# Kernel optimization log

Hardware: AMD Instinct MI355X
Metric: run time of the kernel (lower is better)

The kernel has to match this reference:

```python
import jax, jax.numpy as jnp
import numpy as np
import math

L = 2          # gnn_num_layers
NDIM = 256     # gnn_hidden_size
H = 8          # num_heads
HH = H // 2    # heads per (full, local) split
DK = NDIM // H # 32, also == edim (relation_share_heads)
EDIM = DK
B, NPB = 32, 128
N = B * NPB            # 4096 nodes
EF = B * NPB * NPB     # 524288 complete-graph edges
EL = 131072            # local-graph edges
ELG = 262144           # line-graph edges
R = 128                # relation vocab


def _ln(x, g, b, eps=1e-5):
    m = x.mean(-1, keepdims=True)
    v = ((x - m) ** 2).mean(-1, keepdims=True)
    return (x - m) / jnp.sqrt(v + eps) * g + b


def _ffn(x, W1, b1, W2, b2, g, b):
    h = jax.nn.relu(x @ W1 + b1)
    return _ln(x + h @ W2 + b2, g, b)


def _edge_attn(q, k, v, e, src, dst, n_seg):
    """Relation-aware graph attention (DGL propagate_attention + edge_softmax).
    q,k,v: [n_seg,h,d]; e: [E,h,d] edge-relation bias or None; src,dst: [E].
    score_e = ((k[src]+e) . q[dst]) / sqrt(d); softmax over in-edges of dst;
    out[dst] = sum alpha_e * (v[src]+e)."""
    ks = k[src] + e if e is not None else k[src]          # [E,h,d]
    vs = v[src] + e if e is not None else v[src]          # [E,h,d]
    s = jnp.einsum('ehd,ehd->eh', ks, q[dst]) / math.sqrt(q.shape[-1])
    smax = jax.ops.segment_max(s, dst, num_segments=n_seg)
    ex = jnp.exp(s - jnp.maximum(smax, -1e30)[dst])
    den = jax.ops.segment_sum(ex, dst, num_segments=n_seg)[dst]
    alpha = ex / jnp.where(den > 0, den, 1.0)
    return jax.ops.segment_sum(alpha[..., None] * vs, dst, num_segments=n_seg)


def _model(x, rel_embed,
           n_Wq, n_bq, n_Wk, n_bk, n_Wv, n_bv, n_Wo, n_bo, n_ln_g, n_ln_b,
           n_f_W1, n_f_b1, n_f_W2, n_f_b2, n_f_ln_g, n_f_ln_b,
           e_Wsrc, e_Wdst, e_Wq, e_bq, e_Wk, e_Wv, e_Wo, e_bo, e_ln_g, e_ln_b,
           e_f_W1, e_f_b1, e_f_W2, e_f_b2, e_f_ln_g, e_f_ln_b,
           full_src, full_dst, g_src, g_dst, lg_src, lg_dst, edge_feat, full_edge_feat):
    lg_x = rel_embed[edge_feat]            # [EL, EDIM]  (shared embedding)
    lg_x_full = rel_embed[full_edge_feat]  # [EF, EDIM]  (fixed across layers)
    n, el, ef = x.shape[0], lg_x.shape[0], lg_x_full.shape[0]
    for i in range(L):
        # ---------- node update: first HH heads on full graph, last HH on local ----------
        q = (x @ n_Wq[i] + n_bq[i]).reshape(n, H, DK)
        k = (x @ n_Wk[i] + n_bk[i]).reshape(n, H, DK)
        v = (x @ n_Wv[i] + n_bv[i]).reshape(n, H, DK)
        # edim == d_k -> relation bias broadcast across heads (the expand branch)
        e_full = jnp.broadcast_to(lg_x_full[:, None, :], (ef, HH, DK))
        e_loc = jnp.broadcast_to(lg_x[:, None, :], (el, HH, DK))
        o1 = _edge_attn(q[:, :HH], k[:, :HH], v[:, :HH], e_full, full_src, full_dst, n)
        o2 = _edge_attn(q[:, HH:], k[:, HH:], v[:, HH:], e_loc, g_src, g_dst, n)
        o = jnp.concatenate([o1, o2], axis=1).reshape(n, NDIM)
        x_new = _ln(x + o @ n_Wo[i] + n_bo[i], n_ln_g[i], n_ln_b[i])
        x_new = _ffn(x_new, n_f_W1[i], n_f_b1[i], n_f_W2[i], n_f_b2[i], n_f_ln_g[i], n_f_ln_b[i])
        # ---------- edge update on line graph, conditioned on PRE-update src/dst node feats ----------
        mixed = lg_x + x[g_src] @ e_Wsrc[i] + x[g_dst] @ e_Wdst[i]  # [EL, EDIM]
        dke = EDIM // H
        eq = (mixed @ e_Wq[i] + e_bq[i]).reshape(el, H, dke)
        ek = (mixed @ e_Wk[i]).reshape(el, H, dke)
        ev = (mixed @ e_Wv[i]).reshape(el, H, dke)
        ow = _edge_attn(eq, ek, ev, None, lg_src, lg_dst, el).reshape(el, EDIM)
        lg_new = _ln(lg_x + ow @ e_Wo[i] + e_bo[i], e_ln_g[i], e_ln_b[i])
        lg_new = _ffn(lg_new, e_f_W1[i], e_f_b1[i], e_f_W2[i], e_f_b2[i], e_f_ln_g[i], e_f_ln_b[i])
        x, lg_x = x_new, lg_new
    return x, lg_x


def setup_inputs() -> dict:
    key = jax.random.key(0)
    ki = iter(jax.random.split(key, 48))
    def p(shape, scale=0.05):
        return jax.random.normal(next(ki), shape, dtype=jnp.float32) * scale
    rng = np.random.default_rng(0)
    blk = (np.arange(B, dtype=np.int32) * NPB)
    ii, jj = np.meshgrid(np.arange(NPB, dtype=np.int32), np.arange(NPB, dtype=np.int32), indexing='ij')
    full_src = (blk[:, None, None] + ii[None]).reshape(-1)   # block-diagonal complete graph
    full_dst = (blk[:, None, None] + jj[None]).reshape(-1)
    epb = EL // B
    g_src = (np.repeat(blk, epb) + rng.integers(0, NPB, EL)).astype(np.int32)
    g_dst = (np.repeat(blk, epb) + rng.integers(0, NPB, EL)).astype(np.int32)
    lpb = ELG // B
    eblk = np.arange(B, dtype=np.int32) * epb
    lg_src = (np.repeat(eblk, lpb) + rng.integers(0, epb, ELG)).astype(np.int32)
    lg_dst = (np.repeat(eblk, lpb) + rng.integers(0, epb, ELG)).astype(np.int32)
    return dict(
        x=jax.random.normal(next(ki), (N, NDIM), dtype=jnp.float32),
        rel_embed=p((R, EDIM), 1.0),
        full_src=jnp.asarray(full_src), full_dst=jnp.asarray(full_dst),
        g_src=jnp.asarray(g_src), g_dst=jnp.asarray(g_dst),
        lg_src=jnp.asarray(lg_src), lg_dst=jnp.asarray(lg_dst),
        edge_feat=jnp.asarray(rng.integers(0, R, EL).astype(np.int32)),
        full_edge_feat=jnp.asarray(rng.integers(0, R, EF).astype(np.int32)),
        n_Wq=p((L, NDIM, NDIM)), n_bq=p((L, NDIM)),
        n_Wk=p((L, NDIM, NDIM)), n_bk=p((L, NDIM)),
        n_Wv=p((L, NDIM, NDIM)), n_bv=p((L, NDIM)),
        n_Wo=p((L, NDIM, NDIM)), n_bo=p((L, NDIM)),
        n_ln_g=jnp.ones((L, NDIM), jnp.float32), n_ln_b=jnp.zeros((L, NDIM), jnp.float32),
        n_f_W1=p((L, NDIM, 4 * NDIM)), n_f_b1=p((L, 4 * NDIM)),
        n_f_W2=p((L, 4 * NDIM, NDIM)), n_f_b2=p((L, NDIM)),
        n_f_ln_g=jnp.ones((L, NDIM), jnp.float32), n_f_ln_b=jnp.zeros((L, NDIM), jnp.float32),
        e_Wsrc=p((L, NDIM, EDIM)), e_Wdst=p((L, NDIM, EDIM)),
        e_Wq=p((L, EDIM, EDIM)), e_bq=p((L, EDIM)),
        e_Wk=p((L, EDIM, EDIM)), e_Wv=p((L, EDIM, EDIM)),
        e_Wo=p((L, EDIM, EDIM)), e_bo=p((L, EDIM)),
        e_ln_g=jnp.ones((L, EDIM), jnp.float32), e_ln_b=jnp.zeros((L, EDIM), jnp.float32),
        e_f_W1=p((L, EDIM, 4 * EDIM)), e_f_b1=p((L, 4 * EDIM)),
        e_f_W2=p((L, 4 * EDIM, EDIM)), e_f_b2=p((L, EDIM)),
        e_f_ln_g=jnp.ones((L, EDIM), jnp.float32), e_f_ln_b=jnp.zeros((L, EDIM), jnp.float32),
    )


def reference(x, rel_embed, full_src, full_dst, g_src, g_dst, lg_src, lg_dst,
              edge_feat, full_edge_feat,
              n_Wq, n_bq, n_Wk, n_bk, n_Wv, n_bv, n_Wo, n_bo, n_ln_g, n_ln_b,
              n_f_W1, n_f_b1, n_f_W2, n_f_b2, n_f_ln_g, n_f_ln_b,
              e_Wsrc, e_Wdst, e_Wq, e_bq, e_Wk, e_Wv, e_Wo, e_bo, e_ln_g, e_ln_b,
              e_f_W1, e_f_b1, e_f_W2, e_f_b2, e_f_ln_g, e_f_ln_b):
    return _model(x, rel_embed,
                  n_Wq, n_bq, n_Wk, n_bk, n_Wv, n_bv, n_Wo, n_bo, n_ln_g, n_ln_b,
                  n_f_W1, n_f_b1, n_f_W2, n_f_b2, n_f_ln_g, n_f_ln_b,
                  e_Wsrc, e_Wdst, e_Wq, e_bq, e_Wk, e_Wv, e_Wo, e_bo, e_ln_g, e_ln_b,
                  e_f_W1, e_f_b1, e_f_W2, e_f_b2, e_f_ln_g, e_f_ln_b,
                  full_src, full_dst, g_src, g_dst, lg_src, lg_dst, edge_feat, full_edge_feat)
```

## Files before the change

kernel.cpp:

```cpp
#include <hip/hip_runtime.h>
#include <hip/hip_bf16.h>

typedef __hip_bfloat16 bf16;
typedef unsigned short ush;

static constexpr int kN   = 4096;
static constexpr int kND  = 256;
static constexpr int kEL  = 131072;
static constexpr int kED  = 32;
static constexpr int kELG = 262144;
static constexpr int kL   = 2;
static constexpr int kQW  = 832;
static constexpr float kScaleN = 0.17677669529663687f;

using frag_ab = __attribute__((ext_vector_type(8))) short;
using frag_cd = __attribute__((ext_vector_type(4))) float;

__device__ __forceinline__ float ldf(const void* p, size_t i, int isbf){
    return isbf ? __bfloat162float(((const bf16*)p)[i]) : ((const float*)p)[i];
}
__device__ __forceinline__ ush f2b(float f){ bf16 h = __float2bfloat16(f); return *(ush*)&h; }
__device__ __forceinline__ float b2f(ush u){ return __uint_as_float(((unsigned)u)<<16); }
__device__ __forceinline__ ush ldb(const void* p, size_t i, int isbf){
    return isbf ? ((const ush*)p)[i] : f2b(((const float*)p)[i]);
}

__global__ void detect_k(const ush* __restrict__ xin, int* __restrict__ flag){
    if (threadIdx.x == 0 && blockIdx.x == 0) {
        int plausible = 0;
        for (int i = 0; i < 128; ++i) {
            ush u = xin[i];
            int e = (u >> 7) & 0xFF;
            if (e == 0 || (e >= 110 && e <= 140)) ++plausible;
        }
        *flag = (plausible >= 102) ? 1 : 0;
    }
}

__global__ void setup_misc_k(const void* __restrict__ xin, const void* __restrict__ rel,
                             const int* __restrict__ feat,
                             const void* __restrict__ bq, const void* __restrict__ bk,
                             const void* __restrict__ bv,
                             float* __restrict__ xA, float* __restrict__ lgA,
                             float* __restrict__ bQKV,
                             int* __restrict__ cntL, int* __restrict__ cntG,
                             const int* __restrict__ flag){
    const int isbf = *flag;
    long g = (long)blockIdx.x*256 + threadIdx.x;
    if (g < (long)kN*kND) { xA[g] = ldf(xin, g, isbf); return; }
    g -= (long)kN*kND;
    if (g < (long)kEL*kED) { int e = (int)(g >> 5), d = (int)(g & 31);
        lgA[g] = ldf(rel, (size_t)feat[e]*kED + d, isbf); return; }
    g -= (long)kEL*kED;
    if (g < 2*kQW) {
        int layer = (int)(g / kQW), j = (int)(g - (long)layer*kQW);
        float v = 0.f;
        if (j < 768) { int w = j >> 8, jj = j & 255;
            const void* B = (w==0)?bq:((w==1)?bk:bv);
            v = ldf(B, (size_t)layer*256 + jj, isbf); }
        bQKV[g] = v; return;
    }
    g -= 2*kQW;
    if (g < kN) { cntL[g] = 0; return; }
    g -= kN;
    if (g < kEL) { cntG[g] = 0; return; }
}

__global__ void trans_all_k(
    const void* __restrict__ nWq, const void* __restrict__ nWk, const void* __restrict__ nWv,
    const void* __restrict__ nWo, const void* __restrict__ nF1, const void* __restrict__ nF2,
    const void* __restrict__ eWs, const void* __restrict__ eWd,
    const void* __restrict__ eWq, const void* __restrict__ eWk, const void* __restrict__ eWv,
    const void* __restrict__ eWo, const void* __restrict__ eF1, const void* __restrict__ eF2,
    const int* __restrict__ flag,
    ush* __restrict__ wtQKVSD, ush* __restrict__ wtO, ush* __restrict__ wtF1,
    ush* __restrict__ wtF2, ush* __restrict__ wtEQKV, ush* __restrict__ wtEO,
    ush* __restrict__ wtEF1, ush* __restrict__ wtEF2)
{
    const int isbf = *flag;
    int g = blockIdx.x*256 + threadIdx.x;
    if (g < 393216){
        int w = g >> 17, gg = g & 131071;
        int layer = gg >> 16, idx = gg & 65535;
        int n = idx >> 8, k = idx & 255;
        const void* W = (w==0)?nWq:((w==1)?nWk:nWv);
        wtQKVSD[(size_t)layer*212992 + (size_t)(w*256+n)*256 + k] =
            ldb(W, (size_t)layer*65536 + (size_t)k*256 + n, isbf);
        return;
    }
    g -= 393216;
    if (g < 32768){
        int w = g >> 14, gg = g & 16383;
        int layer = gg >> 13, idx = gg & 8191;
        int n = idx >> 8, k = idx & 255;
        const void* W = w ? eWd : eWs;
        wtQKVSD[(size_t)layer*212992 + (size_t)(768 + w*32 + n)*256 + k] =
            ldb(W, (size_t)layer*8192 + (size_t)k*32 + n, isbf);
        return;
    }
    g -= 32768;
    if (g < 131072){
        int layer = g >> 16, rem = g & 65535;
        int n = rem >> 8, k = rem & 255;
        wtO[g] = ldb(nWo, (size_t)layer*65536 + (size_t)k*256 + n, isbf);
        return;
    }
    g -= 131072;
    if (g < 524288){
        int layer = g >> 18, rem = g & 262143;
        int n = rem >> 8, k = rem & 255;
        wtF1[g] = ldb(nF1, (size_t)layer*262144 + (size_t)k*1024 + n, isbf);
        return;
    }
    g -= 524288;
    if (g < 524288){
        int layer = g >> 18, rem = g & 262143;
        int n = rem >> 10, k = rem & 1023;
        wtF2[g] = ldb(nF2, (size_t)layer*262144 + (size_t)k*256 + n, isbf);
        return;
    }
    g -= 524288;
    if (g < 6144){
        int w = g >> 11, gg = g & 2047;
        int layer = gg >> 10, rem = gg & 1023;
        int n = rem >> 5, k = rem & 31;
        const void* W = (w==0)?eWq:((w==1)?eWk:eWv);
        wtEQKV[g] = ldb(W, (size_t)layer*1024 + (size_t)k*32 + n, isbf);
        return;
    }
    g -= 6144;
    if (g < 2048){
        int layer = g >> 10, rem = g & 1023;
        int n = rem >> 5, k = rem & 31;
        wtEO[g] = ldb(eWo, (size_t)layer*1024 + (size_t)k*32 + n, isbf);
        return;
    }
    g -= 2048;
    if (g < 8192){
        int layer = g >> 12, rem = g & 4095;
        int n = rem >> 5, k = rem & 31;
        wtEF1[g] = ldb(eF1, (size_t)layer*4096 + (size_t)k*128 + n, isbf);
        return;
    }
    g -= 8192;
    if (g < 8192){
        int layer = g >> 12, rem = g & 4095;
        int n = rem >> 7, k = rem & 127;
        wtEF2[g] = ldb(eF2, (size_t)layer*4096 + (size_t)k*32 + n, isbf);
        return;
    }
}

__global__ void count2_k(const int* __restrict__ gd, const int* __restrict__ lgd,
                         int* __restrict__ cntL, int* __restrict__ cntG){
    int g = blockIdx.x*256 + threadIdx.x;
    if (g < kEL) atomicAdd(&cntL[gd[g]], 1);
    else if (g < kEL + kELG) atomicAdd(&cntG[lgd[g - kEL]], 1);
}
__global__ __launch_bounds__(256) void scan_blk2_k(
    const int* __restrict__ cntL, const int* __restrict__ cntG,
    int* __restrict__ rowL, int* __restrict__ rowG, int* __restrict__ bsum)
{
    __shared__ int s[256];
    const int t = threadIdx.x;
    const bool isL = blockIdx.x < 4;
    const int* cnt = isL ? cntL : cntG;
    int* out = isL ? rowL : rowG;
    const int blk = isL ? blockIdx.x : blockIdx.x - 4;
    const int n = isL ? kN : kEL;
    const int b0 = blk*1024;
    int v[4], pre[4], tsum = 0;
    #pragma unroll
    for (int j=0;j<4;++j){
        int idx = b0 + t*4 + j;
        v[j] = (idx < n) ? cnt[idx] : 0;
        pre[j] = tsum; tsum += v[j];
    }
    s[t] = tsum; __syncthreads();
    for (int off=1; off<256; off<<=1){
        int x = (t>=off) ? s[t-off] : 0;
        __syncthreads();
        s[t] += x;
        __syncthreads();
    }
    int texc = s[t] - tsum;
    #pragma unroll
    for (int j=0;j<4;++j){
        int idx = b0 + t*4 + j;
        if (idx < n) out[idx] = texc + pre[j];
    }
    if (t == 255) bsum[(isL ? 0 : 8) + blk] = s[255];
}
__global__ __launch_bounds__(256) void scan_top2_k(int* __restrict__ bsum){
    __shared__ int sL[256], sG[256];
    const int t = threadIdx.x;
    int vL = (t < 4)   ? bsum[t]     : 0;
    int vG = (t < 128) ? bsum[8 + t] : 0;
    sL[t] = vL; sG[t] = vG; __syncthreads();
    for (int off=1; off<256; off<<=1){
        int xL = (t>=off) ? sL[t-off] : 0;
        int xG = (t>=off) ? sG[t-off] : 0;
        __syncthreads();
        sL[t] += xL; sG[t] += xG;
        __syncthreads();
    }
    if (t < 4)   bsum[t]     = sL[t] - vL;
    if (t < 128) bsum[8 + t] = sG[t] - vG;
}
__global__ void scan_add2_k(int* __restrict__ rowL, int* __restrict__ rowG,
                            const int* __restrict__ bsum,
                            int* __restrict__ curL, int* __restrict__ curG){
    int g = blockIdx.x*256 + threadIdx.x;
    if (g < kN){ int v = rowL[g] + bsum[g >> 10]; rowL[g] = v; curL[g] = v; }
    else if (g < kN + kEL){ int gg = g - kN;
        int v = rowG[gg] + bsum[8 + (gg >> 10)]; rowG[gg] = v; curG[gg] = v; }
    if (g == 0){ rowL[kN] = kEL; rowG[kEL] = kELG; }
}
__global__ void fill2_k(const int* __restrict__ gd, const int* __restrict__ lgd,
                        int* __restrict__ curL, int* __restrict__ curG,
                        int* __restrict__ eidL, int* __restrict__ eidG){
    int g = blockIdx.x*256 + threadIdx.x;
    if (g < kEL){ int pos = atomicAdd(&curL[gd[g]], 1); eidL[pos] = g; }
    else if (g < kEL + kELG){ int gg = g - kEL;
        int pos = atomicAdd(&curG[lgd[gg]], 1); eidG[pos] = gg; }
}

__global__ __launch_bounds__(256) void mgemm_k(
    const float* __restrict__ A, const ush* __restrict__ WT,
    const void* __restrict__ bias, size_t boff,
    float* __restrict__ C, const int* __restrict__ flag,
    int M, int N, int K, int flags)
{
    __shared__ __align__(16) ush As[64*40];
    __shared__ __align__(16) ush Ws[64*40];
    const int isbf = *flag;
    const int t = threadIdx.x;
    const int m0 = blockIdx.y*64, n0 = blockIdx.x*64;
    const int wave = t>>6, lane = t&63;
    const int quad = lane>>4, l15 = lane&15;
    const int r = t>>2, kq = (t&3)*8;
    const bool abf = flags & 32;

    frag_cd acc[4];
    #pragma unroll
    for (int tl=0; tl<4; ++tl)
        #pragma unroll
        for (int j=0;j<4;++j) acc[tl][j] = 0.f;

    const float* aprow = A + (size_t)(m0+r)*K + kq;
    const ush*   abrow = (const ush*)A + (size_t)(m0+r)*K + kq;
    const bool wok = (n0 + r) < N;
    const ush* wprow = WT + (size_t)(n0 + (wok ? r : 0))*K + kq;

    float4 a0, a1; uint4 av; uint4 wv;
    auto loadT = [&](int kk){
        if (abf) av = *(const uint4*)(abrow + kk);
        else { a0 = *(const float4*)(aprow + kk); a1 = *(const float4*)(aprow + kk + 4); }
        wv = wok ? *(const uint4*)(wprow + kk) : make_uint4(0u,0u,0u,0u);
    };
    loadT(0);

    for (int kk = 0; kk < K; kk += 32) {
        if (abf) {
            *(uint4*)&As[r*40 + kq] = av;
        } else {
            ushort4 p0 = make_ushort4(f2b(a0.x), f2b(a0.y), f2b(a0.z), f2b(a0.w));
            ushort4 p1 = make_ushort4(f2b(a1.x), f2b(a1.y), f2b(a1.z), f2b(a1.w));
            *(ushort4*)&As[r*40 + kq]     = p0;
            *(ushort4*)&As[r*40 + kq + 4] = p1;
        }
        *(uint4*)&Ws[r*40 + kq] = wv;
        __syncthreads();
        if (kk + 32 < K) loadT(kk + 32);
        frag_ab af = *(const frag_ab*)&As[(wave*16 + l15)*40 + quad*8];
        #pragma unroll
        for (int tl = 0; tl < 4; ++tl) {
            frag_ab bf = *(const frag_ab*)&Ws[(tl*16 + l15)*40 + quad*8];
            acc[tl] = __builtin_amdgcn_mfma_f32_16x16x32_bf16(af, bf, acc[tl], 0, 0, 0);
        }
        __syncthreads();
    }
    const bool do_relu = flags & 2;
    const bool has_b   = flags & 4;
    const bool obf     = flags & 8;
    #pragma unroll
    for (int tl = 0; tl < 4; ++tl) {
        int col = n0 + tl*16 + l15;
        if (col < N) {
            float bv = 0.f;
            if (has_b) bv = (flags & 16) ? ((const float*)bias)[boff + col]
                                         : ldf(bias, boff + col, isbf);
            #pragma unroll
            for (int rg = 0; rg < 4; ++rg) {
                int row = m0 + wave*16 + quad*4 + rg;
                float v = acc[tl][rg] + bv;
                if (do_relu) v = fmaxf(v, 0.f);
                if (obf) ((ush*)C)[(size_t)row*N + col] = f2b(v);
                else     C[(size_t)row*N + col] = v;
            }
        }
    }
}

__global__ __launch_bounds__(64) void ln_k(
    const float* __restrict__ a, const float* __restrict__ b,
    const void* __restrict__ g, const void* __restrict__ be, size_t goff,
    float* __restrict__ out, const int* __restrict__ flag, int D)
{
    const int isbf = *flag;
    const int row = blockIdx.x;
    const int t = threadIdx.x;
    float v[4];
    int cnt = 0;
    float s = 0.f;
    for (int i = t; i < D; i += 64) {
        float x = a[(size_t)row*D + i];
        if (b) x += b[(size_t)row*D + i];
        v[cnt++] = x; s += x;
    }
    #pragma unroll
    for (int off = 32; off > 0; off >>= 1) s += __shfl_down(s, off);
    s = __shfl(s, 0);
    const float mean = s / D;
    float qq = 0.f;
    for (int c2 = 0; c2 < cnt; ++c2) { float d = v[c2]-mean; qq += d*d; }
    #pragma unroll
    for (int off = 32; off > 0; off >>= 1) qq += __shfl_down(qq, off);
    qq = __shfl(qq, 0);
    const float inv = rsqrtf(fmaxf(qq, 0.f) / D + 1e-5f);
    cnt = 0;
    for (int i = t; i < D; i += 64)
        out[(size_t)row*D + i] = (v[cnt++] - mean)*inv*ldf(g, goff + i, isbf) + ldf(be, goff + i, isbf);
}

__global__ __launch_bounds__(256) void eqkv_mfma_k(
    const float* __restrict__ lg, const float* __restrict__ xsd,
    const int* __restrict__ gsrc, const int* __restrict__ gdst,
    const ush* __restrict__ WQKV, size_t woff,
    const void* __restrict__ bq, size_t boff,
    ush* __restrict__ eq, ush* __restrict__ ek, ush* __restrict__ ev,
    const int* __restrict__ flag)
{
    __shared__ __align__(16) ush mixs[128*40];
    __shared__ __align__(16) ush wts[3][32*40];
    __shared__ float bqs[32];
    const int isbf = *flag;
    const int t = threadIdx.x;
    const int e0 = blockIdx.x * 128;
    #pragma unroll
    for (int i = t; i < 768; i += 256) {
        int m = i >> 8, r2 = i & 255;
        int n = r2 >> 3, k4 = (r2 & 7) * 4;
        *(ushort4*)&wts[m][n*40 + k4] =
            *(const ushort4*)&WQKV[(size_t)m*2048 + woff + (size_t)n*32 + k4];
    }
    if (t < 32) bqs[t] = ldf(bq, boff + t, isbf);
    {
        int r = t >> 1, c0 = (t & 1) * 16;
        int e = e0 + r;
        int s = gsrc[e], d2 = gdst[e];
        const float* lp = lg + (size_t)e*32 + c0;
        const float* sp = xsd + (size_t)s*kQW + c0;
        const float* dp = xsd + (size_t)d2*kQW + 32 + c0;
        #pragma unroll
        for (int j = 0; j < 16; ++j)
            mixs[r*40 + c0 + j] = f2b(lp[j] + sp[j] + dp[j]);
    }
    __syncthreads();
    const int wave = t >> 6, l15 = t & 15, quad = (t >> 4) & 3;
    #pragma unroll
    for (int mi = 0; mi < 2; ++mi) {
        const int mt = wave*2 + mi;
        frag_ab af = *(const frag_ab*)&mixs[(mt*16 + l15)*40 + quad*8];
        #pragma unroll
        for (int w = 0; w < 3; ++w) {
            ush* outp = (w==0) ? eq : ((w==1) ? ek : ev);
            #pragma unroll
            for (int nt = 0; nt < 2; ++nt) {
                frag_ab bf = *(const frag_ab*)&wts[w][(nt*16 + l15)*40 + quad*8];
                frag_cd acc = {0.f, 0.f, 0.f, 0.f};
                acc = __builtin_amdgcn_mfma_f32_16x16x32_bf16(af, bf, acc, 0, 0, 0);
                const float bv = (w==0) ? bqs[nt*16 + l15] : 0.f;
                #pragma unroll
                for (int rg = 0; rg < 4; ++rg) {
                    int row = e0 + mt*16 + quad*4 + rg;
                    outp[(size_t)row*32 + nt*16 + l15] = f2b(acc[rg] + bv);
                }
            }
        }
    }
}

__global__ __launch_bounds__(256) void effn_mfma_k(
    const float* __restrict__ A,
    const ush* __restrict__ W1T, size_t w1off, const void* __restrict__ b1, size_t b1off,
    const ush* __restrict__ W2T, size_t w2off, const void* __restrict__ b2, size_t b2off,
    const void* __restrict__ g, const void* __restrict__ be, size_t goff,
    float* __restrict__ out, const int* __restrict__ flag)
{
    __shared__ __align__(16) ush w1t[128*40];
    __shared__ __align__(16) ush w2t[32*136];
    __shared__ __align__(16) ush hid[64*136];
    __shared__ float b1s[128], b2s[32];
    const int isbf = *flag;
    const int t = threadIdx.x;
    const int wave = t >> 6, l15 = t & 15, quad = (t >> 4) & 3;

    #pragma unroll
    for (int i = t; i < 1024; i += 256) {
        int n1 = i >> 3, k4 = (i & 7) * 4;
        *(ushort4*)&w1t[n1*40 + k4] = *(const ushort4*)&W1T[w1off + (size_t)n1*32 + k4];
        int n2 = i >> 5, kq2 = (i & 31) * 4;
        *(ushort4*)&w2t[n2*136 + kq2] = *(const ushort4*)&W2T[w2off + (size_t)n2*128 + kq2];
    }
    if (t < 128) b1s[t] = ldf(b1, b1off + t, isbf);
    if (t < 32)  b2s[t] = ldf(b2, b2off + t, isbf);
    __syncthreads();

    const float g0  = ldf(g,  goff + l15, isbf),      g1v = ldf(g,  goff + 16 + l15, isbf);
    const float be0 = ldf(be, goff + l15, isbf),      be1 = ldf(be, goff + 16 + l15, isbf);
    const float bb0 = b2s[l15], bb1 = b2s[16 + l15];

    for (int tt = 0; tt < 2; ++tt) {
        const int e0 = (blockIdx.x*2 + tt) * 64;
        {
            const int m = wave*16 + l15;
            float4 a0 = *(const float4*)&A[(size_t)(e0+m)*32 + quad*8];
            float4 a1 = *(const float4*)&A[(size_t)(e0+m)*32 + quad*8 + 4];
            ush tmp[8] = {f2b(a0.x),f2b(a0.y),f2b(a0.z),f2b(a0.w),
                          f2b(a1.x),f2b(a1.y),f2b(a1.z),f2b(a1.w)};
            frag_ab af = *(frag_ab*)tmp;
            #pragma unroll
            for (int nt = 0; nt < 8; ++nt) {
                frag_ab bf = *(const frag_ab*)&w1t[(nt*16 + l15)*40 + quad*8];
                frag_cd acc = {0.f, 0.f, 0.f, 0.f};
                acc = __builtin_amdgcn_mfma_f32_16x16x32_bf16(af, bf, acc, 0, 0, 0);
                float bv = b1s[nt*16 + l15];
                #pragma unroll
                for (int rg = 0; rg < 4; ++rg) {
                    int row = wave*16 + quad*4 + rg;
                    hid[row*136 + nt*16 + l15] = f2b(fmaxf(acc[rg] + bv, 0.f));
                }
            }
        }
        frag_cd acc2[2] = {{0.f,0.f,0.f,0.f},{0.f,0.f,0.f,0.f}};
        #pragma unroll
        for (int ks = 0; ks < 4; ++ks) {
            frag_ab af2 = *(const frag_ab*)&hid[(wave*16 + l15)*136 + ks*32 + quad*8];
            #pragma unroll
            for (int tl = 0; tl < 2; ++tl) {
                frag_ab bf2 = *(const frag_ab*)&w2t[(tl*16 + l15)*136 + ks*32 + quad*8];
                acc2[tl] = __builtin_amdgcn_mfma_f32_16x16x32_bf16(af2, bf2, acc2[tl], 0, 0, 0);
            }
        }
        #pragma unroll
        for (int rg = 0; rg < 4; ++rg) {
            const int row = e0 + wave*16 + quad*4 + rg;
            float v0 = acc2[0][rg] + bb0 + A[(size_t)row*32 + l15];
            float v1 = acc2[1][rg] + bb1 + A[(size_t)row*32 + 16 + l15];
            float s = v0 + v1;
            s += __shfl_xor(s,1); s += __shfl_xor(s,2); s += __shfl_xor(s,4); s += __shfl_xor(s,8);
            const float mean = s * (1.f/32.f);
            float q = (v0-mean)*(v0-mean) + (v1-mean)*(v1-mean);
            q += __shfl_xor(q,1); q += __shfl_xor(q,2); q += __shfl_xor(q,4); q += __shfl_xor(q,8);
            const float inv = rsqrtf(q * (1.f/32.f) + 1e-5f);
            out[(size_t)row*32 + l15]      = (v0-mean)*inv*g0  + be0;
            out[(size_t)row*32 + 16 + l15] = (v1-mean)*inv*g1v + be1;
        }
    }
}

__global__ __launch_bounds__(512) void full_attn_k(
    const float* __restrict__ q, const float* __restrict__ k, const float* __restrict__ v,
    const void* __restrict__ rel, const int* __restrict__ feat, float* __restrict__ o,
    const int* __restrict__ flag, int ldq)
{
    __shared__ __align__(8) ush ks[128][36];
    __shared__ __align__(8) ush vs[128][36];
    __shared__ __align__(8) ush rs[128][36];
    __shared__ float pb[8][32][34];
    const int isbf = *flag;
    const int bid = blockIdx.x;
    const int b = bid >> 4, h = (bid >> 2) & 3, qtr = bid & 3;
    const int t = threadIdx.x;
    for (int i = t; i < 4096; i += 512) {
        int r = i >> 5, d = i & 31;
        rs[r][d] = ldb(rel, i, isbf);
        size_t base = ((size_t)(b*128 + r))*ldq + h*32 + d;
        ks[r][d] = f2b(k[base]);
        vs[r][d] = f2b(v[base]);
    }
    __syncthreads();
    const int wave = t >> 6, lane = t & 63;
    const int dstL = lane >> 1, part = lane & 1;
    const int dst = qtr*32 + dstL;
    const int dbase = part*16;
    float qr[16];
    { size_t base = ((size_t)(b*128 + dst))*ldq + h*32 + dbase;
      #pragma unroll
      for (int d=0; d<16; ++d) qr[d] = q[base + d]; }
    const int* fp = feat + (size_t)b*16384 + dst;
    const int s0 = wave*16;
    float m = -1e30f, l = 0.f;
    float acc[16];
    #pragma unroll
    for (int d=0; d<16; ++d) acc[d] = 0.f;
    int f = fp[s0*128];
    for (int sI = 0; sI < 16; ++sI) {
        const int s = s0 + sI;
        int fn = (sI+1 < 16) ? fp[(s+1)*128] : 0;
        float er[16];
        float scp = 0.f;
        #pragma unroll
        for (int j2 = 0; j2 < 4; ++j2) {
            ushort4 eu = *(const ushort4*)&rs[f][dbase + j2*4];
            ushort4 ku = *(const ushort4*)&ks[s][dbase + j2*4];
            float e0 = b2f(eu.x), e1 = b2f(eu.y), e2 = b2f(eu.z), e3 = b2f(eu.w);
            er[j2*4+0]=e0; er[j2*4+1]=e1; er[j2*4+2]=e2; er[j2*4+3]=e3;
            scp += (b2f(ku.x)+e0)*qr[j2*4+0] + (b2f(ku.y)+e1)*qr[j2*4+1]
                 + (b2f(ku.z)+e2)*qr[j2*4+2] + (b2f(ku.w)+e3)*qr[j2*4+3];
        }
        const float sc = (scp + __shfl_xor(scp, 1)) * kScaleN;
        float mn = fmaxf(m, sc);
        float c0 = __expf(m - mn);
        float pp = __expf(sc - mn);
        l = l*c0 + pp;
        #pragma unroll
        for (int j2 = 0; j2 < 4; ++j2) {
            ushort4 vu = *(const ushort4*)&vs[s][dbase + j2*4];
            acc[j2*4+0] = acc[j2*4+0]*c0 + pp*(b2f(vu.x)+er[j2*4+0]);
            acc[j2*4+1] = acc[j2*4+1]*c0 + pp*(b2f(vu.y)+er[j2*4+1]);
            acc[j2*4+2] = acc[j2*4+2]*c0 + pp*(b2f(vu.z)+er[j2*4+2]);
            acc[j2*4+3] = acc[j2*4+3]*c0 + pp*(b2f(vu.w)+er[j2*4+3]);
        }
        m = mn; f = fn;
    }
    if (part == 0) { pb[wave][dstL][0] = m; pb[wave][dstL][1] = l; }
    #pragma unroll
    for (int d=0; d<16; ++d) pb[wave][dstL][2 + dbase + d] = acc[d];
    __syncthreads();
    {
        const int dstL2 = t & 31, grp = t >> 5;
        float mw[8], lw[8];
        #pragma unroll
        for (int w=0; w<8; ++w){ mw[w]=pb[w][dstL2][0]; lw[w]=pb[w][dstL2][1]; }
        float M = mw[0];
        #pragma unroll
        for (int w=1; w<8; ++w) M = fmaxf(M, mw[w]);
        float sw[8];
        float L = 0.f;
        #pragma unroll
        for (int w=0; w<8; ++w){ sw[w] = __expf(mw[w]-M); L += lw[w]*sw[w]; }
        const float inv = 1.f / fmaxf(L, 1e-30f);
        size_t base = ((size_t)(b*128 + qtr*32 + dstL2))*kND + h*32 + grp*2;
        #pragma unroll
        for (int d=0; d<2; ++d) {
            float a = 0.f;
            #pragma unroll
            for (int w=0; w<8; ++w) a += pb[w][dstL2][2+grp*2+d]*sw[w];
            o[base + d] = a*inv;
        }
    }
}

__global__ __launch_bounds__(256) void loc_gather_k(
    const float* __restrict__ q, const float* __restrict__ k, const float* __restrict__ v,
    const float* __restrict__ lg, const int* __restrict__ gsrc,
    const int* __restrict__ rowp, const int* __restrict__ eidl,
    float* __restrict__ o, int ldq)
{
    const int n = blockIdx.x;
    const int h = threadIdx.x >> 6;
    const int lane = threadIdx.x & 63;
    const int g = lane >> 4;
    const int d0 = (lane & 15) * 2;
    const size_t hoff = (size_t)(4 + h) * 32 + d0;
    const float2 q2 = *(const float2*)&q[(size_t)n*ldq + hoff];
    const int beg = rowp[n], end = rowp[n+1];
    const int deg = end - beg;
    float m = -1e30f, l = 0.f, ax = 0.f, ay = 0.f;
    if (deg > 0) {
        const int nIter = (deg + 3) >> 2;
        int idx = beg + g;
        int ce = eidl[min(idx, end-1)];
        int cs = gsrc[ce];
        for (int it = 0; it < nIter; ++it) {
            const bool valid = idx < end;
            const int e = ce, s = cs;
            idx += 4;
            if (it + 1 < nIter) { ce = eidl[min(idx, end-1)]; cs = gsrc[ce]; }
            const float2 kv = *(const float2*)&k[(size_t)s*ldq + hoff];
            const float2 lv = *(const float2*)&lg[(size_t)e*32 + d0];
            const float2 vv = *(const float2*)&v[(size_t)s*ldq + hoff];
            float part = (kv.x+lv.x)*q2.x + (kv.y+lv.y)*q2.y;
            part += __shfl_xor(part, 1);
            part += __shfl_xor(part, 2);
            part += __shfl_xor(part, 4);
            part += __shfl_xor(part, 8);
            const float sc = part * kScaleN;
            const float mn = valid ? fmaxf(m, sc) : m;
            const float c  = __expf(m - mn);
            const float pp = valid ? __expf(sc - mn) : 0.f;
            l  = l*c  + pp;
            ax = ax*c + pp*(vv.x+lv.x);
            ay = ay*c + pp*(vv.y+lv.y);
            m  = mn;
        }
        #pragma unroll
        for (int off = 16; off <= 32; off <<= 1) {
            const float mo = __shfl_xor(m, off);
            const float lo = __shfl_xor(l, off);
            const float xo = __shfl_xor(ax, off);
            const float yo = __shfl_xor(ay, off);
            const float M  = fmaxf(m, mo);
            const float c1 = __expf(m - M);
            const float c2 = __expf(mo - M);
            l  = l*c1  + lo*c2;
            ax = ax*c1 + xo*c2;
            ay = ay*c1 + yo*c2;
            m  = M;
        }
    }
    if (g == 0) {
        const float inv = 1.f / fmaxf(l, 1e-30f);
        *(float2*)&o[(size_t)n*kND + hoff] = make_float2(ax*inv, ay*inv);
    }
}

__global__ __launch_bounds__(256) void lgs_ewo_k(
    const ush* __restrict__ eq, const ush* __restrict__ ek, const ush* __restrict__ ev,
    const int* __restrict__ lsrc, const int* __restrict__ rowp, const int* __restrict__ eidl,
    const float* __restrict__ res,
    const ush* __restrict__ WO, size_t wooff, const void* __restrict__ bo, size_t booff,
    const void* __restrict__ g1, const void* __restrict__ be1, size_t g1off,
    float* __restrict__ out, const int* __restrict__ flag)
{
    __shared__ __align__(16) ush ows[32*40];
    __shared__ __align__(16) ush wos[32*40];
    __shared__ float cs[32][36];
    __shared__ float bos[32], gs[32], bs[32];
    const int isbf = *flag;
    const int t = threadIdx.x;
    const int base = blockIdx.x * 32;
    {
        int n = t >> 3, k4 = (t & 7) * 4;
        *(ushort4*)&wos[n*40 + k4] = *(const ushort4*)&WO[wooff + (size_t)n*32 + k4];
    }
    if (t < 32) {
        bos[t] = ldf(bo, booff + t, isbf);
        gs[t]  = ldf(g1, g1off + t, isbf);
        bs[t]  = ldf(be1, g1off + t, isbf);
    }
    {
        const int d2 = base + (t >> 3), h = t & 7;
        const ushort4 qu = *(const ushort4*)&eq[(size_t)d2*32 + h*4];
        const float q0 = b2f(qu.x), q1 = b2f(qu.y), q2 = b2f(qu.z), q3 = b2f(qu.w);
        const int beg = rowp[d2], end = rowp[d2+1];
        float m = -1e30f, l = 0.f;
        float4 acc = make_float4(0.f,0.f,0.f,0.f);
        int i = beg;
        int s = 0;
        if (i < end) { s = lsrc[eidl[i]]; }
        while (i < end) {
            const int sc_s = s;
            ++i;
            if (i < end) { s = lsrc[eidl[i]]; }
            const ushort4 ku = *(const ushort4*)&ek[(size_t)sc_s*32 + h*4];
            const ushort4 vu = *(const ushort4*)&ev[(size_t)sc_s*32 + h*4];
            float sc = (b2f(ku.x)*q0 + b2f(ku.y)*q1 + b2f(ku.z)*q2 + b2f(ku.w)*q3) * 0.5f;
            float mn = fmaxf(m, sc);
            float c = __expf(m - mn);
            float pp = __expf(sc - mn);
            l = l*c + pp;
            acc.x = acc.x*c + pp*b2f(vu.x);
            acc.y = acc.y*c + pp*b2f(vu.y);
            acc.z = acc.z*c + pp*b2f(vu.z);
            acc.w = acc.w*c + pp*b2f(vu.w);
            m = mn;
        }
        const float inv = 1.f / fmaxf(l, 1e-30f);
        const int r = t >> 3, c0 = h*4;
        ows[r*40 + c0 + 0] = f2b(acc.x*inv);
        ows[r*40 + c0 + 1] = f2b(acc.y*inv);
        ows[r*40 + c0 + 2] = f2b(acc.z*inv);
        ows[r*40 + c0 + 3] = f2b(acc.w*inv);
    }
    __syncthreads();
    {
        const int wave = t >> 6, l15 = t & 15, quad = (t >> 4) & 3;
        const int mt = wave & 1, nt = wave >> 1;
        frag_ab af = *(const frag_ab*)&ows[(mt*16 + l15)*40 + quad*8];
        frag_ab bf = *(const frag_ab*)&wos[(nt*16 + l15)*40 + quad*8];
        frag_cd acc = {0.f, 0.f, 0.f, 0.f};
        acc = __builtin_amdgcn_mfma_f32_16x16x32_bf16(af, bf, acc, 0, 0, 0);
        #pragma unroll
        for (int rg = 0; rg < 4; ++rg) {
            const int row = mt*16 + quad*4 + rg;
            const int col = nt*16 + l15;
            cs[row][col] = acc[rg] + bos[col] + res[(size_t)(base+row)*32 + col];
        }
    }
    __syncthreads();
    {
        const int row = t >> 3, c0 = (t & 7) * 4;
        const float v0 = cs[row][c0], v1 = cs[row][c0+1];
        const float v2 = cs[row][c0+2], v3 = cs[row][c0+3];
        float s = v0+v1+v2+v3;
        s += __shfl_xor(s,1); s += __shfl_xor(s,2); s += __shfl_xor(s,4);
        const float mean = s * (1.f/32.f);
        float qq = (v0-mean)*(v0-mean)+(v1-mean)*(v1-mean)
                 + (v2-mean)*(v2-mean)+(v3-mean)*(v3-mean);
        qq += __shfl_xor(qq,1); qq += __shfl_xor(qq,2); qq += __shfl_xor(qq,4);
        const float inv = rsqrtf(qq * (1.f/32.f) + 1e-5f);
        float o0 = (v0-mean)*inv*gs[c0+0] + bs[c0+0];
        float o1 = (v1-mean)*inv*gs[c0+1] + bs[c0+1];
        float o2 = (v2-mean)*inv*gs[c0+2] + bs[c0+2];
        float o3 = (v3-mean)*inv*gs[c0+3] + bs[c0+3];
        *(float4*)&out[(size_t)(base+row)*32 + c0] = make_float4(o0,o1,o2,o3);
    }
}

__global__ void out_k(const float* __restrict__ xf, const float* __restrict__ lgf,
                      void* __restrict__ out, const int* __restrict__ flag){
    const int isbf = *flag;
    int g = blockIdx.x*256 + threadIdx.x;
    float v = (g < kN*kND) ? xf[g] : lgf[g - kN*kND];
    if (isbf) ((bf16*)out)[g] = __float2bfloat16(v);
    else      ((float*)out)[g] = v;
}

static inline void mgemm(const float* A, const ush* WT, const void* bias, size_t boff,
                         float* C, const int* flag, int M, int N, int K, int flags,
                         hipStream_t s){
    dim3 grid((N+63)/64, M/64);
    mgemm_k<<<grid, 256, 0, s>>>(A, WT, bias, boff, C, flag, M, N, K, flags);
}

extern "C" void kernel_launch(void* const* d_in, const int* in_sizes, int n_in,
                              void* d_out, int out_size, void* d_ws, size_t ws_size,
                              hipStream_t stream) {
    const void* x_in      = d_in[0];
    const void* rel       = d_in[1];
    const int* g_src      = (const int*)d_in[4];
    const int* g_dst      = (const int*)d_in[5];
    const int* lg_src     = (const int*)d_in[6];
    const int* lg_dst     = (const int*)d_in[7];
    const int* edge_feat  = (const int*)d_in[8];
    const int* full_feat  = (const int*)d_in[9];
    const void* n_Wq   = d_in[10];
    const void* n_bq   = d_in[11];
    const void* n_Wk   = d_in[12];
    const void* n_bk   = d_in[13];
    const void* n_Wv   = d_in[14];
    const void* n_bv   = d_in[15];
    const void* n_Wo   = d_in[16];
    const void* n_bo   = d_in[17];
    const void* n_lng  = d_in[18];
    const void* n_lnb  = d_in[19];
    const void* n_fW1  = d_in[20];
    const void* n_fb1  = d_in[21];
    const void* n_fW2  = d_in[22];
    const void* n_fb2  = d_in[23];
    const void* n_flng = d_in[24];
    const void* n_flnb = d_in[25];
    const void* e_Wsrc = d_in[26];
    const void* e_Wdst = d_in[27];
    const void* e_Wq   = d_in[28];
    const void* e_bq   = d_in[29];
    const void* e_Wk   = d_in[30];
    const void* e_Wv   = d_in[31];
    const void* e_Wo   = d_in[32];
    const void* e_bo   = d_in[33];
    const void* e_lng  = d_in[34];
    const void* e_lnb  = d_in[35];
    const void* e_fW1  = d_in[36];
    const void* e_fb1  = d_in[37];
    const void* e_fW2  = d_in[38];
    const void* e_fb2  = d_in[39];
    const void* e_flng = d_in[40];
    const void* e_flnb = d_in[41];

    float* p = (float*)d_ws;
    size_t off = 0;
    auto AL = [&](size_t n){ float* r = p + off; off += n; return r; };
    int* flagp = (int*)AL(64);
    float* xA   = AL((size_t)kN*kND);
    float* xB   = AL((size_t)kN*kND);
    float* xM   = AL((size_t)kN*kND);
    float* qkvb = AL((size_t)kN*kQW);
    float* ob   = AL((size_t)kN*kND);
    float* tN   = AL((size_t)kN*kND);
    ush*   nh   = (ush*)AL((size_t)kN*512);
    float* lgA  = AL((size_t)kEL*kED);
    float* lgB  = AL((size_t)kEL*kED);
    float* lgM  = AL((size_t)kEL*kED);
    ush*   eqb  = (ush*)AL((size_t)kEL*16);
    ush*   ekb  = (ush*)AL((size_t)kEL*16);
    ush*   evb  = (ush*)AL((size_t)kEL*16);
    int* cntL  = (int*)AL(kN);
    int* rowL  = (int*)AL(kN + 64);
    int* curL  = (int*)AL(kN);
    int* eidL  = (int*)AL(kEL);
    int* cntG  = (int*)AL(kEL);
    int* rowG  = (int*)AL(kEL + 64);
    int* curG  = (int*)AL(kEL);
    int* eidG  = (int*)AL(kELG);
    int* bsum  = (int*)AL(256);
    ush* wtQKVSD = (ush*)AL(212992);
    float* bQKV  = AL(2*kQW);
    ush* wtO  = (ush*)AL(65536);
    ush* wtF1 = (ush*)AL(262144);
    ush* wtF2 = (ush*)AL(262144);
    ush* wtEQKV = (ush*)AL(3072);
    ush* wtEO   = (ush*)AL(1024);
    ush* wtEF1  = (ush*)AL(4096);
    ush* wtEF2  = (ush*)AL(4096);
    if (ws_size < off * sizeof(float)) return;

    detect_k<<<1, 64, 0, stream>>>((const ush*)x_in, flagp);
    {
        long total = (long)kN*kND + (long)kEL*kED + 2*kQW + kN + kEL;
        int blocks = (int)((total + 255) / 256);
        setup_misc_k<<<blocks, 256, 0, stream>>>(x_in, rel, edge_feat, n_bq, n_bk, n_bv,
                                                 xA, lgA, bQKV, cntL, cntG, flagp);
    }
    trans_all_k<<<6368, 256, 0, stream>>>(n_Wq, n_Wk, n_Wv, n_Wo, n_fW1, n_fW2,
                                          e_Wsrc, e_Wdst, e_Wq, e_Wk, e_Wv, e_Wo,
                                          e_fW1, e_fW2, flagp,
                                          wtQKVSD, wtO, wtF1, wtF2,
                                          wtEQKV, wtEO, wtEF1, wtEF2);

    count2_k<<<(kEL+kELG)/256, 256, 0, stream>>>(g_dst, lg_dst, cntL, cntG);
    scan_blk2_k<<<132, 256, 0, stream>>>(cntL, cntG, rowL, rowG, bsum);
    scan_top2_k<<<1, 256, 0, stream>>>(bsum);
    scan_add2_k<<<(kN+kEL)/256, 256, 0, stream>>>(rowL, rowG, bsum, curL, curG);
    fill2_k<<<(kEL+kELG)/256, 256, 0, stream>>>(g_dst, lg_dst, curL, curG, eidL, eidG);

    float* xc = xA;  float* xn = xB;
    float* lgc = lgA; float* lgn = lgB;

    for (int i = 0; i < kL; ++i) {
        const size_t o256 = (size_t)i*kND;
        const size_t o1024= (size_t)i*1024;
        const size_t o32  = (size_t)i*kED;
        const size_t o128 = (size_t)i*128;

        mgemm(xc, wtQKVSD + (size_t)i*212992, bQKV, (size_t)i*kQW, qkvb, flagp,
              kN, kQW, kND, 4|16, stream);
        full_attn_k<<<512, 512, 0, stream>>>(qkvb, qkvb+256, qkvb+512, rel, full_feat,
                                             ob, flagp, kQW);
        loc_gather_k<<<kN, 256, 0, stream>>>(qkvb, qkvb+256, qkvb+512, lgc, g_src,
                                             rowL, eidL, ob, kQW);
        mgemm(ob, wtO + (size_t)i*65536, n_bo, o256, tN, flagp, kN, kND, kND, 4, stream);
        ln_k<<<kN, 64, 0, stream>>>(xc, tN, n_lng, n_lnb, o256, xM, flagp, kND);
        mgemm(xM, wtF1 + (size_t)i*262144, n_fb1, o1024, (float*)nh, flagp,
              kN, 1024, kND, 4|2|8, stream);
        mgemm((const float*)nh, wtF2 + (size_t)i*262144, n_fb2, o256, tN, flagp,
              kN, kND, 1024, 4|32, stream);
        ln_k<<<kN, 64, 0, stream>>>(xM, tN, n_flng, n_flnb, o256, xn, flagp, kND);

        eqkv_mfma_k<<<kEL/128, 256, 0, stream>>>(lgc, qkvb + 768, g_src, g_dst,
                                                 wtEQKV, (size_t)i*1024, e_bq, o32,
                                                 eqb, ekb, evb, flagp);
        lgs_ewo_k<<<kEL/32, 256, 0, stream>>>(eqb, ekb, evb, lg_src, rowG, eidG,
                                              lgc, wtEO, (size_t)i*1024, e_bo, o32,
                                              e_lng, e_lnb, o32, lgM, flagp);
        effn_mfma_k<<<kEL/128, 256, 0, stream>>>(lgM, wtEF1, (size_t)i*4096, e_fb1, o128,
                                                 wtEF2, (size_t)i*4096, e_fb2, o32,
                                                 e_flng, e_flnb, o32, lgn, flagp);

        { float* t = xc; xc = xn; xn = t; }
        { float* t = lgc; lgc = lgn; lgn = t; }
    }

    out_k<<<(kN*kND + kEL*kED)/256, 256, 0, stream>>>(xc, lgc, d_out, flagp);
}
```

Measured before the change: 579.6 us.

## Store edge features and GEMM A-operands as bf16 to halve memory traffic

Edge-feature buffers (lg, lgM) and the attention output are now kept in bf16 rather than fp32. The layernorm kernels also write a bf16 copy of their output, so the node GEMMs can read bf16 A operands directly through the flag-32 path instead of converting fp32 on load. This cuts global memory bytes read and written across many kernels. The cost is extra rounding of the residual edge state across layers, which could affect accuracy.

```diff
diff --git a/kernel.cpp b/kernel.cpp
--- a/kernel.cpp
+++ b/kernel.cpp
@@ -41,16 +41,21 @@
                              const int* __restrict__ feat,
                              const void* __restrict__ bq, const void* __restrict__ bk,
                              const void* __restrict__ bv,
-                             float* __restrict__ xA, float* __restrict__ lgA,
+                             float* __restrict__ xA, ush* __restrict__ xAb,
+                             ush* __restrict__ lgA,
                              float* __restrict__ bQKV,
                              int* __restrict__ cntL, int* __restrict__ cntG,
                              const int* __restrict__ flag){
     const int isbf = *flag;
     long g = (long)blockIdx.x*256 + threadIdx.x;
-    if (g < (long)kN*kND) { xA[g] = ldf(xin, g, isbf); return; }
+    if (g < (long)kN*kND) {
+        float v = ldf(xin, g, isbf);
+        xA[g] = v; xAb[g] = f2b(v);
+        return;
+    }
     g -= (long)kN*kND;
     if (g < (long)kEL*kED) { int e = (int)(g >> 5), d = (int)(g & 31);
-        lgA[g] = ldf(rel, (size_t)feat[e]*kED + d, isbf); return; }
+        lgA[g] = ldb(rel, (size_t)feat[e]*kED + d, isbf); return; }
     g -= (long)kEL*kED;
     if (g < 2*kQW) {
         int layer = (int)(g / kQW), j = (int)(g - (long)layer*kQW);
@@ -305,7 +310,8 @@
 __global__ __launch_bounds__(64) void ln_k(
     const float* __restrict__ a, const float* __restrict__ b,
     const void* __restrict__ g, const void* __restrict__ be, size_t goff,
-    float* __restrict__ out, const int* __restrict__ flag, int D)
+    float* __restrict__ out, ush* __restrict__ outb,
+    const int* __restrict__ flag, int D)
 {
     const int isbf = *flag;
     const int row = blockIdx.x;
@@ -329,12 +335,15 @@
     qq = __shfl(qq, 0);
     const float inv = rsqrtf(fmaxf(qq, 0.f) / D + 1e-5f);
     cnt = 0;
-    for (int i = t; i < D; i += 64)
-        out[(size_t)row*D + i] = (v[cnt++] - mean)*inv*ldf(g, goff + i, isbf) + ldf(be, goff + i, isbf);
+    for (int i = t; i < D; i += 64) {
+        float r = (v[cnt++] - mean)*inv*ldf(g, goff + i, isbf) + ldf(be, goff + i, isbf);
+        out[(size_t)row*D + i] = r;
+        outb[(size_t)row*D + i] = f2b(r);
+    }
 }
 
 __global__ __launch_bounds__(256) void eqkv_mfma_k(
-    const float* __restrict__ lg, const float* __restrict__ xsd,
+    const ush* __restrict__ lg, const float* __restrict__ xsd,
     const int* __restrict__ gsrc, const int* __restrict__ gdst,
     const ush* __restrict__ WQKV, size_t woff,
     const void* __restrict__ bq, size_t boff,
@@ -359,12 +368,12 @@
         int r = t >> 1, c0 = (t & 1) * 16;
         int e = e0 + r;
         int s = gsrc[e], d2 = gdst[e];
-        const float* lp = lg + (size_t)e*32 + c0;
+        const ush* lp = lg + (size_t)e*32 + c0;
         const float* sp = xsd + (size_t)s*kQW + c0;
         const float* dp = xsd + (size_t)d2*kQW + 32 + c0;
         #pragma unroll
         for (int j = 0; j < 16; ++j)
-            mixs[r*40 + c0 + j] = f2b(lp[j] + sp[j] + dp[j]);
+            mixs[r*40 + c0 + j] = f2b(b2f(lp[j]) + sp[j] + dp[j]);
     }
     __syncthreads();
     const int wave = t >> 6, l15 = t & 15, quad = (t >> 4) & 3;
@@ -392,11 +401,11 @@
 }
 
 __global__ __launch_bounds__(256) void effn_mfma_k(
-    const float* __restrict__ A,
+    const ush* __restrict__ A,
     const ush* __restrict__ W1T, size_t w1off, const void* __restrict__ b1, size_t b1off,
     const ush* __restrict__ W2T, size_t w2off, const void* __restrict__ b2, size_t b2off,
     const void* __restrict__ g, const void* __restrict__ be, size_t goff,
-    float* __restrict__ out, const int* __restrict__ flag)
+    ush* __restrict__ out, const int* __restrict__ flag)
 {
     __shared__ __align__(16) ush w1t[128*40];
     __shared__ __align__(16) ush w2t[32*136];
@@ -425,11 +434,7 @@
         const int e0 = (blockIdx.x*2 + tt) * 64;
         {
             const int m = wave*16 + l15;
-            float4 a0 = *(const float4*)&A[(size_t)(e0+m)*32 + quad*8];
-            float4 a1 = *(const float4*)&A[(size_t)(e0+m)*32 + quad*8 + 4];
-            ush tmp[8] = {f2b(a0.x),f2b(a0.y),f2b(a0.z),f2b(a0.w),
-                          f2b(a1.x),f2b(a1.y),f2b(a1.z),f2b(a1.w)};
-            frag_ab af = *(frag_ab*)tmp;
+            frag_ab af = *(const frag_ab*)&A[(size_t)(e0+m)*32 + quad*8];
             #pragma unroll
             for (int nt = 0; nt < 8; ++nt) {
                 frag_ab bf = *(const frag_ab*)&w1t[(nt*16 + l15)*40 + quad*8];
@@ -456,23 +461,23 @@
         #pragma unroll
         for (int rg = 0; rg < 4; ++rg) {
             const int row = e0 + wave*16 + quad*4 + rg;
-            float v0 = acc2[0][rg] + bb0 + A[(size_t)row*32 + l15];
-            float v1 = acc2[1][rg] + bb1 + A[(size_t)row*32 + 16 + l15];
+            float v0 = acc2[0][rg] + bb0 + b2f(A[(size_t)row*32 + l15]);
+            float v1 = acc2[1][rg] + bb1 + b2f(A[(size_t)row*32 + 16 + l15]);
             float s = v0 + v1;
             s += __shfl_xor(s,1); s += __shfl_xor(s,2); s += __shfl_xor(s,4); s += __shfl_xor(s,8);
             const float mean = s * (1.f/32.f);
             float q = (v0-mean)*(v0-mean) + (v1-mean)*(v1-mean);
             q += __shfl_xor(q,1); q += __shfl_xor(q,2); q += __shfl_xor(q,4); q += __shfl_xor(q,8);
             const float inv = rsqrtf(q * (1.f/32.f) + 1e-5f);
-            out[(size_t)row*32 + l15]      = (v0-mean)*inv*g0  + be0;
-            out[(size_t)row*32 + 16 + l15] = (v1-mean)*inv*g1v + be1;
+            out[(size_t)row*32 + l15]      = f2b((v0-mean)*inv*g0  + be0);
+            out[(size_t)row*32 + 16 + l15] = f2b((v1-mean)*inv*g1v + be1);
         }
     }
 }
 
 __global__ __launch_bounds__(512) void full_attn_k(
     const float* __restrict__ q, const float* __restrict__ k, const float* __restrict__ v,
-    const void* __restrict__ rel, const int* __restrict__ feat, float* __restrict__ o,
+    const void* __restrict__ rel, const int* __restrict__ feat, ush* __restrict__ o,
     const int* __restrict__ flag, int ldq)
 {
     __shared__ __align__(8) ush ks[128][36];
@@ -558,16 +563,16 @@
             float a = 0.f;
             #pragma unroll
             for (int w=0; w<8; ++w) a += pb[w][dstL2][2+grp*2+d]*sw[w];
-            o[base + d] = a*inv;
+            o[base + d] = f2b(a*inv);
         }
     }
 }
 
 __global__ __launch_bounds__(256) void loc_gather_k(
     const float* __restrict__ q, const float* __restrict__ k, const float* __restrict__ v,
-    const float* __restrict__ lg, const int* __restrict__ gsrc,
+    const ush* __restrict__ lg, const int* __restrict__ gsrc,
     const int* __restrict__ rowp, const int* __restrict__ eidl,
-    float* __restrict__ o, int ldq)
+    ush* __restrict__ o, int ldq)
 {
     const int n = blockIdx.x;
     const int h = threadIdx.x >> 6;
@@ -590,9 +595,10 @@
             idx += 4;
             if (it + 1 < nIter) { ce = eidl[min(idx, end-1)]; cs = gsrc[ce]; }
             const float2 kv = *(const float2*)&k[(size_t)s*ldq + hoff];
-            const float2 lv = *(const float2*)&lg[(size_t)e*32 + d0];
+            const ushort2 lvu = *(const ushort2*)&lg[(size_t)e*32 + d0];
             const float2 vv = *(const float2*)&v[(size_t)s*ldq + hoff];
-            float part = (kv.x+lv.x)*q2.x + (kv.y+lv.y)*q2.y;
+            const float lvx = b2f(lvu.x), lvy = b2f(lvu.y);
+            float part = (kv.x+lvx)*q2.x + (kv.y+lvy)*q2.y;
             part += __shfl_xor(part, 1);
             part += __shfl_xor(part, 2);
             part += __shfl_xor(part, 4);
@@ -602,8 +608,8 @@
             const float c  = __expf(m - mn);
             const float pp = valid ? __expf(sc - mn) : 0.f;
             l  = l*c  + pp;
-            ax = ax*c + pp*(vv.x+lv.x);
-            ay = ay*c + pp*(vv.y+lv.y);
+            ax = ax*c + pp*(vv.x+lvx);
+            ay = ay*c + pp*(vv.y+lvy);
             m  = mn;
         }
         #pragma unroll
@@ -623,17 +629,17 @@
     }
     if (g == 0) {
         const float inv = 1.f / fmaxf(l, 1e-30f);
-        *(float2*)&o[(size_t)n*kND + hoff] = make_float2(ax*inv, ay*inv);
+        *(ushort2*)&o[(size_t)n*kND + hoff] = make_ushort2(f2b(ax*inv), f2b(ay*inv));
     }
 }
 
 __global__ __launch_bounds__(256) void lgs_ewo_k(
     const ush* __restrict__ eq, const ush* __restrict__ ek, const ush* __restrict__ ev,
     const int* __restrict__ lsrc, const int* __restrict__ rowp, const int* __restrict__ eidl,
-    const float* __restrict__ res,
+    const ush* __restrict__ res,
     const ush* __restrict__ WO, size_t wooff, const void* __restrict__ bo, size_t booff,
     const void* __restrict__ g1, const void* __restrict__ be1, size_t g1off,
-    float* __restrict__ out, const int* __restrict__ flag)
+    ush* __restrict__ out, const int* __restrict__ flag)
 {
     __shared__ __align__(16) ush ows[32*40];
     __shared__ __align__(16) ush wos[32*40];
@@ -697,7 +703,7 @@
         for (int rg = 0; rg < 4; ++rg) {
             const int row = mt*16 + quad*4 + rg;
             const int col = nt*16 + l15;
-            cs[row][col] = acc[rg] + bos[col] + res[(size_t)(base+row)*32 + col];
+            cs[row][col] = acc[rg] + bos[col] + b2f(res[(size_t)(base+row)*32 + col]);
         }
     }
     __syncthreads();
@@ -712,21 +718,26 @@
                  + (v2-mean)*(v2-mean)+(v3-mean)*(v3-mean);
         qq += __shfl_xor(qq,1); qq += __shfl_xor(qq,2); qq += __shfl_xor(qq,4);
         const float inv = rsqrtf(qq * (1.f/32.f) + 1e-5f);
-        float o0 = (v0-mean)*inv*gs[c0+0] + bs[c0+0];
-        float o1 = (v1-mean)*inv*gs[c0+1] + bs[c0+1];
-        float o2 = (v2-mean)*inv*gs[c0+2] + bs[c0+2];
-        float o3 = (v3-mean)*inv*gs[c0+3] + bs[c0+3];
-        *(float4*)&out[(size_t)(base+row)*32 + c0] = make_float4(o0,o1,o2,o3);
-    }
-}
-
-__global__ void out_k(const float* __restrict__ xf, const float* __restrict__ lgf,
+        out[(size_t)(base+row)*32 + c0 + 0] = f2b((v0-mean)*inv*gs[c0+0] + bs[c0+0]);
+        out[(size_t)(base+row)*32 + c0 + 1] = f2b((v1-mean)*inv*gs[c0+1] + bs[c0+1]);
+        out[(size_t)(base+row)*32 + c0 + 2] = f2b((v2-mean)*inv*gs[c0+2] + bs[c0+2]);
+        out[(size_t)(base+row)*32 + c0 + 3] = f2b((v3-mean)*inv*gs[c0+3] + bs[c0+3]);
+    }
+}
+
+__global__ void out_k(const float* __restrict__ xf, const ush* __restrict__ lgf,
                       void* __restrict__ out, const int* __restrict__ flag){
     const int isbf = *flag;
     int g = blockIdx.x*256 + threadIdx.x;
-    float v = (g < kN*kND) ? xf[g] : lgf[g - kN*kND];
-    if (isbf) ((bf16*)out)[g] = __float2bfloat16(v);
-    else      ((float*)out)[g] = v;
+    if (g < kN*kND) {
+        float v = xf[g];
+        if (isbf) ((ush*)out)[g] = f2b(v);
+        else      ((float*)out)[g] = v;
+    } else {
+        ush u = lgf[g - kN*kND];
+        if (isbf) ((ush*)out)[g] = u;
+        else      ((float*)out)[g] = b2f(u);
+    }
 }
 
 static inline void mgemm(const float* A, const ush* WT, const void* bias, size_t boff,
@@ -787,13 +798,16 @@
     float* xA   = AL((size_t)kN*kND);
     float* xB   = AL((size_t)kN*kND);
     float* xM   = AL((size_t)kN*kND);
+    ush*   xAb  = (ush*)AL((size_t)kN*kND/2);
+    ush*   xBb  = (ush*)AL((size_t)kN*kND/2);
+    ush*   xMb  = (ush*)AL((size_t)kN*kND/2);
     float* qkvb = AL((size_t)kN*kQW);
-    float* ob   = AL((size_t)kN*kND);
+    ush*   ob   = (ush*)AL((size_t)kN*kND/2);
     float* tN   = AL((size_t)kN*kND);
     ush*   nh   = (ush*)AL((size_t)kN*512);
-    float* lgA  = AL((size_t)kEL*kED);
-    float* lgB  = AL((size_t)kEL*kED);
-    float* lgM  = AL((size_t)kEL*kED);
+    ush*   lgA  = (ush*)AL((size_t)kEL*kED/2);
+    ush*   lgB  = (ush*)AL((size_t)kEL*kED/2);
+    ush*   lgM  = (ush*)AL((size_t)kEL*kED/2);
     ush*   eqb  = (ush*)AL((size_t)kEL*16);
     ush*   ekb  = (ush*)AL((size_t)kEL*16);
     ush*   evb  = (ush*)AL((size_t)kEL*16);
@@ -822,7 +836,7 @@
         long total = (long)kN*kND + (long)kEL*kED + 2*kQW + kN + kEL;
         int blocks = (int)((total + 255) / 256);
         setup_misc_k<<<blocks, 256, 0, stream>>>(x_in, rel, edge_feat, n_bq, n_bk, n_bv,
-                                                 xA, lgA, bQKV, cntL, cntG, flagp);
+                                                 xA, xAb, lgA, bQKV, cntL, cntG, flagp);
     }
     trans_all_k<<<6368, 256, 0, stream>>>(n_Wq, n_Wk, n_Wv, n_Wo, n_fW1, n_fW2,
                                           e_Wsrc, e_Wdst, e_Wq, e_Wk, e_Wv, e_Wo,
@@ -837,7 +851,8 @@
     fill2_k<<<(kEL+kELG)/256, 256, 0, stream>>>(g_dst, lg_dst, curL, curG, eidL, eidG);
 
     float* xc = xA;  float* xn = xB;
-    float* lgc = lgA; float* lgn = lgB;
+    ush* xcb = xAb;  ush* xnb = xBb;
+    ush* lgc = lgA;  ush* lgn = lgB;
 
     for (int i = 0; i < kL; ++i) {
         const size_t o256 = (size_t)i*kND;
@@ -845,19 +860,20 @@
         const size_t o32  = (size_t)i*kED;
         const size_t o128 = (size_t)i*128;
 
-        mgemm(xc, wtQKVSD + (size_t)i*212992, bQKV, (size_t)i*kQW, qkvb, flagp,
-              kN, kQW, kND, 4|16, stream);
+        mgemm((const float*)xcb, wtQKVSD + (size_t)i*212992, bQKV, (size_t)i*kQW, qkvb,
+              flagp, kN, kQW, kND, 4|16|32, stream);
         full_attn_k<<<512, 512, 0, stream>>>(qkvb, qkvb+256, qkvb+512, rel, full_feat,
                                              ob, flagp, kQW);
         loc_gather_k<<<kN, 256, 0, stream>>>(qkvb, qkvb+256, qkvb+512, lgc, g_src,
                                              rowL, eidL, ob, kQW);
-        mgemm(ob, wtO + (size_t)i*65536, n_bo, o256, tN, flagp, kN, kND, kND, 4, stream);
-        ln_k<<<kN, 64, 0, stream>>>(xc, tN, n_lng, n_lnb, o256, xM, flagp, kND);
-        mgemm(xM, wtF1 + (size_t)i*262144, n_fb1, o1024, (float*)nh, flagp,
-              kN, 1024, kND, 4|2|8, stream);
+        mgemm((const float*)ob, wtO + (size_t)i*65536, n_bo, o256, tN, flagp,
+              kN, kND, kND, 4|32, stream);
+        ln_k<<<kN, 64, 0, stream>>>(xc, tN, n_lng, n_lnb, o256, xM, xMb, flagp, kND);
+        mgemm((const float*)xMb, wtF1 + (size_t)i*262144, n_fb1, o1024, (float*)nh, flagp,
+              kN, 1024, kND, 4|2|8|32, stream);
         mgemm((const float*)nh, wtF2 + (size_t)i*262144, n_fb2, o256, tN, flagp,
               kN, kND, 1024, 4|32, stream);
-        ln_k<<<kN, 64, 0, stream>>>(xM, tN, n_flng, n_flnb, o256, xn, flagp, kND);
+        ln_k<<<kN, 64, 0, stream>>>(xM, tN, n_flng, n_flnb, o256, xn, xnb, flagp, kND);
 
         eqkv_mfma_k<<<kEL/128, 256, 0, stream>>>(lgc, qkvb + 768, g_src, g_dst,
                                                  wtEQKV, (size_t)i*1024, e_bq, o32,
@@ -870,7 +886,8 @@
                                                  e_flng, e_flnb, o32, lgn, flagp);
 
         { float* t = xc; xc = xn; xn = t; }
-        { float* t = lgc; lgc = lgn; lgn = t; }
+        { ush* t = xcb; xcb = xnb; xnb = t; }
+        { ush* t = lgc; lgc = lgn; lgn = t; }
     }
 
     out_k<<<(kN*kND + kEL*kED)/256, 256, 0, stream>>>(xc, lgc, d_out, flagp);
```

After: 564.1 us. 1.03x faster.
